# Optimization experiments

Measured on AMD Instinct MI355X. Metric: run time of the kernel, lower is better.

## Reference

```python
import jax, jax.numpy as jnp
import numpy as np
from jax.scipy.special import digamma, gammaln

NUM_CLASSES = 3
FOCAL_GAMMA = 2.0
LABEL_SMOOTHING = 0.1
EVIDENTIAL_W = 0.1
CONTRASTIVE_W = 0.1
BOUNDARY_W = 0.15
TRIPLET_W = 0.1
QUALITY_W = 0.1
TRIPLET_MARGIN = 1.5


def setup_inputs() -> dict:
    key = jax.random.key(0)
    k1, k2, k3 = jax.random.split(key, 3)
    B, D = 4096, 512
    logits = jax.random.normal(k1, (B, NUM_CLASSES), dtype=jnp.float32)
    targets = jax.random.randint(k2, (B,), 0, 3)
    features = jax.random.normal(k3, (B, D), dtype=jnp.float32)
    alpha = jax.random.uniform(jax.random.fold_in(key, 7), (B, NUM_CLASSES), dtype=jnp.float32)
    focal_alpha = jnp.array([1.0, 2.0, 1.5], dtype=jnp.float32)
    class_weights = jnp.array([1.0, 2.0, 1.5], dtype=jnp.float32)
    return {"logits": logits, "targets": targets, "features": features,
            "alpha": alpha, "epoch": 1, "focal_alpha": focal_alpha,
            "class_weights": class_weights}


def reference(logits, targets, features, alpha, epoch, focal_alpha, class_weights):
    B = logits.shape[0]
    C = NUM_CLASSES

    # ---- focal loss (label-smoothed CE, torch semantics) ----
    logp = jax.nn.log_softmax(logits, axis=1)                      # [B,C]
    nll = -jnp.take_along_axis(logp, targets[:, None], axis=1)[:, 0]
    ce_ls = (1.0 - LABEL_SMOOTHING) * nll + LABEL_SMOOTHING * (-logp.mean(axis=1))
    pt = jnp.exp(-ce_ls)
    focal = (focal_alpha[targets] * (1.0 - pt) ** FOCAL_GAMMA * ce_ls).mean()

    # ---- weighted CE (torch weighted mean: sum(w*nll)/sum(w)) ----
    w = class_weights[targets]
    ce = (w * nll).sum() / w.sum()

    # ---- enhanced boundary loss ----
    probs = jax.nn.softmax(logits, axis=1)
    real = targets == 0
    semi = targets == 1
    syn = targets == 2
    rb = jnp.where(real, probs[:, 1] + 0.6 * probs[:, 2], 0.0).sum()
    sb = jnp.where(syn, probs[:, 1] + 0.4 * probs[:, 0], 0.0).sum()
    mb = jnp.where(semi, 1.0 - probs[:, 1] + 0.3 * (probs[:, 0] + probs[:, 2]), 0.0).sum()
    boundary = (rb + sb + 4.5 * mb) / (B + 1e-8)

    total = 0.4 * focal + 0.3 * ce + BOUNDARY_W * boundary

    # ---- normalized features and pairwise cosine-sim matrix ----
    norms = jnp.linalg.norm(features, axis=1, keepdims=True)
    f = features / jnp.maximum(norms, 1e-12)
    sim = f @ f.T                                                  # [B,B]
    same = targets[:, None] == targets[None, :]
    eye = jnp.eye(B, dtype=bool)

    # ---- enhanced contrastive loss ----
    pos = jnp.where(same, (1.0 - sim) ** 2, 0.0).sum()
    neg = jnp.where(~same, jnp.clip(sim - 0.2, 0.0) ** 2, 0.0).sum()
    semi_pair = semi[:, None] & semi[None, :]
    semi_l = jnp.where(semi_pair, (1.0 - sim) ** 2, 0.0).sum()
    contrastive = (pos + neg + 4.0 * semi_l) / (B * B + 1e-8)

    # ---- enhanced triplet loss (batch-hard, vectorized) ----
    d2 = jnp.clip(2.0 - 2.0 * sim, 0.0)
    dist = jnp.sqrt(jnp.where(eye, 1.0, d2))  # diag masked; safe sqrt
    pos_mask = same & ~eye
    neg_mask = ~same
    hp = jnp.max(jnp.where(pos_mask, dist, -jnp.inf), axis=1)
    hn = jnp.min(jnp.where(neg_mask, dist, jnp.inf), axis=1)
    valid = pos_mask.any(axis=1) & neg_mask.any(axis=1)
    margin = TRIPLET_MARGIN * jnp.where(targets == 1, 2.5, 1.0)
    tl = jax.nn.relu(hp - hn + margin)
    cnt = valid.sum()
    triplet = jnp.where(cnt > 0,
                        jnp.where(valid, tl, 0.0).sum() / jnp.maximum(cnt, 1),
                        0.0)

    # ---- quality-invariant loss (upper-tri same-class pairs) ----
    upper = jnp.triu(jnp.ones((B, B), dtype=bool), k=1)
    qmask = same & upper
    npairs = qmask.sum()
    q = jnp.where(qmask, (1.0 - sim) ** 2, 0.0).sum() / jnp.maximum(npairs, 1)
    frac2 = syn.astype(jnp.float32).mean()
    q = q * jnp.where(syn.sum() > 0, 1.0 + 2.5 * frac2, 1.0)
    quality = jnp.where(npairs > 0, q, 0.0)

    # ---- evidential loss ----
    onehot = jax.nn.one_hot(targets, C, dtype=jnp.float32)
    S = alpha.sum(axis=1, keepdims=True) + 1e-8
    likelihood = (onehot * (digamma(S) - digamma(alpha + 1e-8))).sum(axis=1)
    at = onehot + (1.0 - onehot) * alpha
    ats = at.sum(axis=1) + 1e-8
    kl = (gammaln(ats) - gammaln(at + 1e-8).sum(axis=1)
          + ((at - 1.0) * (digamma(at + 1e-8) - digamma(ats[:, None] + 1e-8))).sum(axis=1))
    annealing = min(1.0, (epoch / 25.0) ** 2)
    evidential = likelihood.mean() + annealing * 0.2 * kl.mean()

    total = (total + CONTRASTIVE_W * contrastive + TRIPLET_W * triplet
             + QUALITY_W * quality + EVIDENTIAL_W * evidential)
    return total
```

## Files before the change

kernel.cpp:

```cpp
#include <hip/hip_runtime.h>
#include <hip/hip_bf16.h>
#include <cstdint>

typedef __attribute__((ext_vector_type(8))) __bf16 bf8;
typedef __attribute__((ext_vector_type(4))) float f32x4;

__device__ __forceinline__ unsigned mapf(float x){
  unsigned u = __float_as_uint(x);
  return (u & 0x80000000u) ? ~u : (u | 0x80000000u);
}
__device__ __forceinline__ float unmapf(unsigned u){
  return __uint_as_float((u & 0x80000000u) ? (u & 0x7FFFFFFFu) : ~u);
}

__device__ float digammaf_(float x){
  float r = 0.f;
  while (x < 6.f){ r -= 1.f/x; x += 1.f; }
  float inv = 1.f/x, inv2 = inv*inv;
  r += logf(x) - 0.5f*inv
     - inv2*(0.08333333333f - inv2*(0.008333333333f - inv2*0.003968253968f));
  return r;
}

__global__ __launch_bounds__(256) void k_prep(const float* __restrict__ feat,
    __bf16* __restrict__ fb2,
    const float* __restrict__ logits, const int* __restrict__ targets,
    const float* __restrict__ alpha,  const float* __restrict__ fa,
    const float* __restrict__ cw, int B, int D,
    float* __restrict__ psum, unsigned* rowMinU, unsigned* rowMaxU){
  int bid = blockIdx.x, tid = threadIdx.x;
  int wave = tid >> 6, lane = tid & 63;

  int row = bid*4 + wave;
  const float* src = feat + (size_t)row*D;
  float ss = 0.f;
  for (int c = lane*4; c < D; c += 64*4){
    float4 v = *(const float4*)(src + c);
    ss += v.x*v.x + v.y*v.y + v.z*v.z + v.w*v.w;
  }
  #pragma unroll
  for (int off=32; off; off>>=1) ss += __shfl_xor(ss, off);
  float inv = 1.f / fmaxf(sqrtf(ss), 1e-12f);

  int p = row >> 6, r = row & 63;
  int mi = r >> 4, l16r = r & 15;
  int NCH = D >> 5;
  for (int c = lane*8; c < D; c += 64*8){
    float4 v0 = *(const float4*)(src + c);
    float4 v1 = *(const float4*)(src + c + 4);
    bf8 o;
    o[0]=(__bf16)(v0.x*inv); o[1]=(__bf16)(v0.y*inv);
    o[2]=(__bf16)(v0.z*inv); o[3]=(__bf16)(v0.w*inv);
    o[4]=(__bf16)(v1.x*inv); o[5]=(__bf16)(v1.y*inv);
    o[6]=(__bf16)(v1.z*inv); o[7]=(__bf16)(v1.w*inv);
    int cc = c >> 5;
    int q  = (c >> 3) & 3;
    size_t off = ((size_t)(p*NCH + cc)*4 + mi)*512 + (q*16 + l16r)*8;
    *(bf8*)(fb2 + off) = o;
  }

  if (tid < 4){ rowMinU[bid*4+tid] = 0xFFFFFFFFu; rowMaxU[bid*4+tid] = 0u; }

  if (wave == 0){
    float r0=0.f,r1=0.f,r2=0.f,r3=0.f,r4=0.f,r5=0.f;
    if (lane < 4){
      int i = bid*4 + lane;
      float l0=logits[3*i], l1=logits[3*i+1], l2=logits[3*i+2];
      int t = targets[i];
      float m = fmaxf(l0, fmaxf(l1,l2));
      float e0=expf(l0-m), e1=expf(l1-m), e2=expf(l2-m);
      float se = e0+e1+e2;
      float lse = m + logf(se);
      float lp0=l0-lse, lp1=l1-lse, lp2=l2-lse;
      float lpt = (t==0)?lp0:((t==1)?lp1:lp2);
      float nll = -lpt;
      float ce_ls = 0.9f*nll + 0.1f*(-(lp0+lp1+lp2)*(1.f/3.f));
      float pt = expf(-ce_ls);
      float om = 1.f - pt;
      float focal_i = fa[t]*om*om*ce_ls;
      float w = cw[t];
      float ce_n = w*nll, ce_d = w;
      float p0=e0/se, p1=e1/se, p2=e2/se;
      float bnd;
      if (t==0)      bnd = p1 + 0.6f*p2;
      else if (t==2) bnd = p1 + 0.4f*p0;
      else           bnd = 4.5f*(1.f - p1 + 0.3f*(p0+p2));
      float a0=alpha[3*i], a1=alpha[3*i+1], a2=alpha[3*i+2];
      float S = a0+a1+a2 + 1e-8f;
      float at_ = (t==0)?a0:((t==1)?a1:a2);
      float lik = digammaf_(S) - digammaf_(at_ + 1e-8f);
      float b0 = (t==0)?1.f:a0, b1 = (t==1)?1.f:a1, b2 = (t==2)?1.f:a2;
      float ats = b0+b1+b2 + 1e-8f;
      float psa = digammaf_(ats + 1e-8f);
      float kl = lgammaf(ats)
         - (lgammaf(b0+1e-8f)+lgammaf(b1+1e-8f)+lgammaf(b2+1e-8f))
         + (b0-1.f)*(digammaf_(b0+1e-8f)-psa)
         + (b1-1.f)*(digammaf_(b1+1e-8f)-psa)
         + (b2-1.f)*(digammaf_(b2+1e-8f)-psa);
      r0=focal_i; r1=ce_n; r2=ce_d; r3=bnd; r4=lik; r5=kl;
    }
    float s0 = ((__shfl(r0,0)+__shfl(r0,1))+__shfl(r0,2))+__shfl(r0,3);
    float s1 = ((__shfl(r1,0)+__shfl(r1,1))+__shfl(r1,2))+__shfl(r1,3);
    float s2 = ((__shfl(r2,0)+__shfl(r2,1))+__shfl(r2,2))+__shfl(r2,3);
    float s3 = ((__shfl(r3,0)+__shfl(r3,1))+__shfl(r3,2))+__shfl(r3,3);
    float s4 = ((__shfl(r4,0)+__shfl(r4,1))+__shfl(r4,2))+__shfl(r4,3);
    float s5 = ((__shfl(r5,0)+__shfl(r5,1))+__shfl(r5,2))+__shfl(r5,3);
    if (lane == 0){
      psum[bid*8+0]=s0; psum[bid*8+1]=s1; psum[bid*8+2]=s2;
      psum[bid*8+3]=s3; psum[bid*8+4]=s4; psum[bid*8+5]=s5;
    }
  }
}

__global__ __launch_bounds__(64, 4) void k_pairs(const __bf16* __restrict__ fb2,
    const int* __restrict__ targets, int B, int D,
    float* __restrict__ pairPart, unsigned* rowMinU, unsigned* rowMaxU){
  int NBY = B >> 5;
  int bid = blockIdx.x;
  int by  = bid % NBY;
  int p   = bid / NBY;
  int bx0 = by + 2*p;
  int lane = threadIdx.x;
  if (bx0 >= NBY){
    if (lane == 0) *(float4*)(pairPart + bid*4) = make_float4(0.f,0.f,0.f,0.f);
    return;
  }
  int bx1 = bx0 + 1;
  bool hasT1 = (bx1 < NBY);
  bool isDiag0 = (bx0 == by);
  int rowBase = by*32, colBase0 = bx0*32, colBase1 = bx1*32;

  int quad = lane >> 4, l16 = lane & 15;
  int NCH = D >> 5;

  const __bf16* pA  = fb2 + ((size_t)(by >>1)*NCH*4 + (by &1)*2)*512 + lane*8;
  const __bf16* pB0 = fb2 + ((size_t)(bx0>>1)*NCH*4 + (bx0&1)*2)*512 + lane*8;
  const __bf16* pB1 = hasT1
      ? fb2 + ((size_t)(bx1>>1)*NCH*4 + (bx1&1)*2)*512 + lane*8
      : pB0;

  int trow = targets[rowBase + (lane & 31)];
  int tcol0[2], tcol1[2];
  tcol0[0] = targets[colBase0 + l16];
  tcol0[1] = targets[colBase0 + 16 + l16];
  tcol1[0] = hasT1 ? targets[colBase1 + l16]      : 0;
  tcol1[1] = hasT1 ? targets[colBase1 + 16 + l16] : 0;

  f32x4 C0[2][2] = {};
  f32x4 C1[2][2] = {};

  #define LD(Ab, B0b, B1b, it) do{ \
    Ab[0]  = *(const bf8*)(pA  + (size_t)(it)*2048); \
    Ab[1]  = *(const bf8*)(pA  + (size_t)(it)*2048 + 512); \
    B0b[0] = *(const bf8*)(pB0 + (size_t)(it)*2048); \
    B0b[1] = *(const bf8*)(pB0 + (size_t)(it)*2048 + 512); \
    B1b[0] = *(const bf8*)(pB1 + (size_t)(it)*2048); \
    B1b[1] = *(const bf8*)(pB1 + (size_t)(it)*2048 + 512); \
  }while(0)

  #define COMP(Ab, B0b, B1b) do{ \
    _Pragma("unroll") \
    for (int mi=0; mi<2; mi++) \
      _Pragma("unroll") \
      for (int ni=0; ni<2; ni++) \
        C0[mi][ni] = __builtin_amdgcn_mfma_f32_16x16x32_bf16(Ab[mi], B0b[ni], C0[mi][ni], 0,0,0); \
    _Pragma("unroll") \
    for (int mi=0; mi<2; mi++) \
      _Pragma("unroll") \
      for (int ni=0; ni<2; ni++) \
        C1[mi][ni] = __builtin_amdgcn_mfma_f32_16x16x32_bf16(Ab[mi], B1b[ni], C1[mi][ni], 0,0,0); \
  }while(0)

  if (NCH == 16){
    bf8 A[3][2], Bb0[3][2], Bb1[3][2];
    LD(A[0], Bb0[0], Bb1[0], 0);
    LD(A[1], Bb0[1], Bb1[1], 1);
    #pragma unroll
    for (int it=0; it<16; ++it){
      if (it+2 < 16) LD(A[(it+2)%3], Bb0[(it+2)%3], Bb1[(it+2)%3], it+2);
      COMP(A[it%3], Bb0[it%3], Bb1[it%3]);
    }
  } else {
    bf8 A0[2], B00[2], B10[2], A1[2], B01[2], B11[2];
    LD(A0, B00, B10, 0);
    for (int it=0; it<NCH; it+=2){
      LD(A1, B01, B11, it+1);
      COMP(A0, B00, B10);
      if (it+2 < NCH) LD(A0, B00, B10, it+2);
      COMP(A1, B01, B11);
    }
  }
  #undef LD
  #undef COMP

  float rowMinReg = 2.f, rowMaxReg = -2.f;
  float posA=0.f, negA=0.f, semiA=0.f, diagA=0.f;
  float posB=0.f, negB=0.f, semiB=0.f, diagB=0.f;

  auto epi = [&](const f32x4 (&Cx)[2][2], const int (&tcolx)[2], int colBasex,
                 bool isD, float& posx, float& negx, float& semix, float& diagx){
    float cmin[2] = {2.f, 2.f}, cmax[2] = {-2.f, -2.f};
    #pragma unroll
    for (int mi=0; mi<2; mi++){
      #pragma unroll
      for (int r=0; r<4; r++){
        int rl = mi*16 + quad*4 + r;
        int row = rowBase + rl;
        int tr = __shfl(trow, rl);
        float vmin = 2.f, vmax = -2.f;
        #pragma unroll
        for (int ni=0; ni<2; ni++){
          int col = colBasex + ni*16 + l16;
          float s = Cx[mi][ni][r];
          if (tr == tcolx[ni]){
            float omv = 1.f - s;
            float q = omv*omv;
            posx += q;
            if (tr == 1) semix += q;
            if (row == col) diagx += q;
            else {
              vmin = fminf(vmin, s);
              cmin[ni] = fminf(cmin[ni], s);
            }
          } else {
            float c0 = fmaxf(s - 0.2f, 0.f);
            negx += c0*c0;
            vmax = fmaxf(vmax, s);
            cmax[ni] = fmaxf(cmax[ni], s);
          }
        }
        #pragma unroll
        for (int off=1; off<16; off<<=1){
          vmin = fminf(vmin, __shfl_xor(vmin, off));
          vmax = fmaxf(vmax, __shfl_xor(vmax, off));
        }
        if (l16 == mi*4 + r){
          rowMinReg = fminf(rowMinReg, vmin);
          rowMaxReg = fmaxf(rowMaxReg, vmax);
        }
      }
    }
    if (!isD){
      #pragma unroll
      for (int ni=0; ni<2; ni++){
        cmin[ni] = fminf(cmin[ni], __shfl_xor(cmin[ni], 16));
        cmin[ni] = fminf(cmin[ni], __shfl_xor(cmin[ni], 32));
        cmax[ni] = fmaxf(cmax[ni], __shfl_xor(cmax[ni], 16));
        cmax[ni] = fmaxf(cmax[ni], __shfl_xor(cmax[ni], 32));
      }
      if (lane < 32){
        float cnv = (lane < 16) ? cmin[0] : cmin[1];
        float cxv = (lane < 16) ? cmax[0] : cmax[1];
        atomicMin(&rowMinU[colBasex + lane], mapf(cnv));
        atomicMax(&rowMaxU[colBasex + lane], mapf(cxv));
      }
    }
  };

  epi(C0, tcol0, colBase0, isDiag0, posA, negA, semiA, diagA);
  if (hasT1) epi(C1, tcol1, colBase1, false, posB, negB, semiB, diagB);

  if (l16 < 8){
    int row = rowBase + quad*4 + (l16 & 3) + 16*(l16 >> 2);
    atomicMin(&rowMinU[row], mapf(rowMinReg));
    atomicMax(&rowMaxU[row], mapf(rowMaxReg));
  }

  float fac0 = isDiag0 ? 1.f : 2.f;
  float pos  = posA*fac0 + posB*2.f;
  float neg  = negA*fac0 + negB*2.f;
  float semi = semiA*fac0 + semiB*2.f;
  float diag = diagA;

  #pragma unroll
  for (int off=32; off; off>>=1){
    pos  += __shfl_xor(pos, off);
    neg  += __shfl_xor(neg, off);
    semi += __shfl_xor(semi, off);
    diag += __shfl_xor(diag, off);
  }
  if (lane == 0)
    *(float4*)(pairPart + bid*4) = make_float4(pos, neg, semi, diag);
}

__global__ __launch_bounds__(1024) void k_final(const int* __restrict__ targets,
    const int* __restrict__ epoch_p, int B, int nprep, int nblk,
    const float* __restrict__ pairPart, const float* __restrict__ psum,
    const unsigned* rowMinU, const unsigned* rowMaxU, float* out){
  int tid = threadIdx.x, wave = tid>>6, lane = tid&63;
  __shared__ float redf[16][8];
  __shared__ int   redi[16][4];
  __shared__ float tot6[6];
  __shared__ int   cns[3];
  __shared__ float ptot[4];

  {
    int c0=0,c1=0,c2=0;
    for (int i4 = tid; i4 < B/4; i4 += 1024){
      int4 tv = ((const int4*)targets)[i4];
      c0 += (tv.x==0)+(tv.y==0)+(tv.z==0)+(tv.w==0);
      c1 += (tv.x==1)+(tv.y==1)+(tv.z==1)+(tv.w==1);
      c2 += (tv.x==2)+(tv.y==2)+(tv.z==2)+(tv.w==2);
    }
    #pragma unroll
    for (int off=32; off; off>>=1){
      c0+=__shfl_xor(c0,off); c1+=__shfl_xor(c1,off); c2+=__shfl_xor(c2,off);
    }
    if (lane==0){ redi[wave][0]=c0; redi[wave][1]=c1; redi[wave][2]=c2; }
  }
  {
    float v0=0,v1=0,v2=0,v3=0,v4=0,v5=0;
    for (int s = tid; s < nprep; s += 1024){
      float4 a = *(const float4*)(psum + s*8);
      float4 b = *(const float4*)(psum + s*8 + 4);
      v0+=a.x; v1+=a.y; v2+=a.z; v3+=a.w; v4+=b.x; v5+=b.y;
    }
    #pragma unroll
    for (int off=32; off; off>>=1){
      v0+=__shfl_xor(v0,off); v1+=__shfl_xor(v1,off); v2+=__shfl_xor(v2,off);
      v3+=__shfl_xor(v3,off); v4+=__shfl_xor(v4,off); v5+=__shfl_xor(v5,off);
    }
    if (lane==0){
      redf[wave][0]=v0; redf[wave][1]=v1; redf[wave][2]=v2;
      redf[wave][3]=v3; redf[wave][4]=v4; redf[wave][5]=v5;
    }
  }
  __syncthreads();
  if (tid == 0){
    int c0=0,c1=0,c2=0;
    float v[6]={0,0,0,0,0,0};
    for (int w2=0; w2<16; w2++){
      c0+=redi[w2][0]; c1+=redi[w2][1]; c2+=redi[w2][2];
      for (int j=0;j<6;j++) v[j]+=redf[w2][j];
    }
    cns[0]=c0; cns[1]=c1; cns[2]=c2;
    for (int j=0;j<6;j++) tot6[j]=v[j];
  }
  __syncthreads();

  {
    float p=0,n=0,s2=0,d=0;
    for (int s = tid; s < nblk; s += 1024){
      float4 a = *(const float4*)(pairPart + s*4);
      p+=a.x; n+=a.y; s2+=a.z; d+=a.w;
    }
    #pragma unroll
    for (int off=32; off; off>>=1){
      p+=__shfl_xor(p,off); n+=__shfl_xor(n,off);
      s2+=__shfl_xor(s2,off); d+=__shfl_xor(d,off);
    }
    if (lane==0){ redf[wave][0]=p; redf[wave][1]=n; redf[wave][2]=s2; redf[wave][3]=d; }
  }
  __syncthreads();
  if (tid == 0){
    float a=0,b=0,c=0,e=0;
    for (int w2=0; w2<16; w2++){ a+=redf[w2][0]; b+=redf[w2][1]; c+=redf[w2][2]; e+=redf[w2][3]; }
    ptot[0]=a; ptot[1]=b; ptot[2]=c; ptot[3]=e;
  }
  __syncthreads();

  int n0=cns[0], n1=cns[1], n2=cns[2];

  float tsum = 0.f, tcnt = 0.f;
  for (int i = tid; i < B; i += 1024){
    int t = targets[i];
    int nt = (t==0)?n0:((t==1)?n1:n2);
    if (nt - 1 > 0 && B - nt > 0){
      float mn = unmapf(rowMinU[i]);
      float mx = unmapf(rowMaxU[i]);
      float hp = sqrtf(fmaxf(2.f - 2.f*mn, 0.f));
      float hn = sqrtf(fmaxf(2.f - 2.f*mx, 0.f));
      float margin = 1.5f * ((t==1) ? 2.5f : 1.f);
      float tl = fmaxf(hp - hn + margin, 0.f);
      tsum += tl; tcnt += 1.f;
    }
  }
  #pragma unroll
  for (int off=32; off; off>>=1){ tsum += __shfl_xor(tsum, off); tcnt += __shfl_xor(tcnt, off); }
  if (lane==0){ redf[wave][6]=tsum; redf[wave][7]=tcnt; }
  __syncthreads();

  if (tid==0){
    float ts=0, tn=0;
    for (int w2=0; w2<16; w2++){ ts+=redf[w2][6]; tn+=redf[w2][7]; }
    float triplet = (tn > 0.f) ? ts / fmaxf(tn, 1.f) : 0.f;
    float pos=ptot[0], neg=ptot[1], semi=ptot[2], diag=ptot[3];
    float Bf = (float)B;
    float focal = tot6[0] / Bf;
    float ce = tot6[1] / tot6[2];
    float boundary = tot6[3] / (Bf + 1e-8f);
    float contrastive = (pos + neg + 4.f*semi) / (Bf*Bf + 1e-8f);
    long long npl = ((long long)n0*(n0-1) + (long long)n1*(n1-1) + (long long)n2*(n2-1))/2;
    float qsum = (pos - diag) * 0.5f;
    float q = qsum / (float)(npl > 0 ? npl : 1);
    if (n2 > 0) q *= (1.f + 2.5f * ((float)n2 / Bf));
    float quality = (npl > 0) ? q : 0.f;
    int ep = epoch_p[0];
    float er = (float)ep / 25.f;
    float ann = fminf(1.f, er*er);
    float evidential = tot6[4]/Bf + ann*0.2f*tot6[5]/Bf;
    float total = 0.4f*focal + 0.3f*ce + 0.15f*boundary
                + 0.1f*contrastive + 0.1f*triplet + 0.1f*quality + 0.1f*evidential;
    out[0] = total;
  }
}

extern "C" void kernel_launch(void* const* d_in, const int* in_sizes, int n_in,
                              void* d_out, int out_size, void* d_ws, size_t ws_size,
                              hipStream_t stream){
  const float* logits   = (const float*)d_in[0];
  const int*   targets  = (const int*)d_in[1];
  const float* features = (const float*)d_in[2];
  const float* alpha    = (const float*)d_in[3];
  const int*   epoch    = (const int*)d_in[4];
  const float* fa       = (const float*)d_in[5];
  const float* cw       = (const float*)d_in[6];
  int B = in_sizes[1];
  int D = in_sizes[2] / B;
  int nprep = B/4;
  int NBY = B / 32;
  int PMAX = (NBY + 1) / 2;
  int nblk = NBY * PMAX;

  char* ws = (char*)d_ws;
  float*    psum     = (float*)(ws);
  float*    pairPart = (float*)(ws + 65536);
  unsigned* rowMinU  = (unsigned*)(ws + 65536 + 196608);
  unsigned* rowMaxU  = (unsigned*)(ws + 65536 + 196608 + (size_t)B*4);
  __bf16*   fb2      = (__bf16*)(ws + 65536 + 196608 + (size_t)B*8);

  k_prep <<<nprep, 256, 0, stream>>>(features, fb2, logits, targets, alpha, fa, cw,
                                     B, D, psum, rowMinU, rowMaxU);
  k_pairs<<<nblk, 64, 0, stream>>>(fb2, targets, B, D, pairPart, rowMinU, rowMaxU);
  k_final<<<1, 1024, 0, stream>>>(targets, epoch, B, nprep, nblk, pairPart, psum,
                                  rowMinU, rowMaxU, (float*)d_out);
}
```

Before: 130.1 us.

## Pack four pair-tile waves per block and drop the triple-buffered D=512 path

The pair kernel now launches 256-thread blocks in which each wave handles one independent tile-pair slot, instead of one 64-thread block per slot. This cuts the block count by four and removes the launch bound that allowed four blocks per CU. The specialised triple-buffered, fully unrolled loop for D=512 is removed, so the generic double-buffered loop runs for every D. The aim is to reduce block-scheduling overhead and register pressure, at the risk of hiding memory latency less well in the main loop.

```diff
diff --git a/kernel.cpp b/kernel.cpp
--- a/kernel.cpp
+++ b/kernel.cpp
@@ -112,17 +112,18 @@
   }
 }
 
-__global__ __launch_bounds__(64, 4) void k_pairs(const __bf16* __restrict__ fb2,
-    const int* __restrict__ targets, int B, int D,
+__global__ __launch_bounds__(256) void k_pairs(const __bf16* __restrict__ fb2,
+    const int* __restrict__ targets, int B, int D, int nslot,
     float* __restrict__ pairPart, unsigned* rowMinU, unsigned* rowMaxU){
   int NBY = B >> 5;
-  int bid = blockIdx.x;
-  int by  = bid % NBY;
-  int p   = bid / NBY;
+  int wave = threadIdx.x >> 6, lane = threadIdx.x & 63;
+  int slot = blockIdx.x*4 + wave;
+  if (slot >= nslot) return;
+  int by  = slot % NBY;
+  int p   = slot / NBY;
   int bx0 = by + 2*p;
-  int lane = threadIdx.x;
   if (bx0 >= NBY){
-    if (lane == 0) *(float4*)(pairPart + bid*4) = make_float4(0.f,0.f,0.f,0.f);
+    if (lane == 0) *(float4*)(pairPart + slot*4) = make_float4(0.f,0.f,0.f,0.f);
     return;
   }
   int bx1 = bx0 + 1;
@@ -171,16 +172,7 @@
         C1[mi][ni] = __builtin_amdgcn_mfma_f32_16x16x32_bf16(Ab[mi], B1b[ni], C1[mi][ni], 0,0,0); \
   }while(0)
 
-  if (NCH == 16){
-    bf8 A[3][2], Bb0[3][2], Bb1[3][2];
-    LD(A[0], Bb0[0], Bb1[0], 0);
-    LD(A[1], Bb0[1], Bb1[1], 1);
-    #pragma unroll
-    for (int it=0; it<16; ++it){
-      if (it+2 < 16) LD(A[(it+2)%3], Bb0[(it+2)%3], Bb1[(it+2)%3], it+2);
-      COMP(A[it%3], Bb0[it%3], Bb1[it%3]);
-    }
-  } else {
+  {
     bf8 A0[2], B00[2], B10[2], A1[2], B01[2], B11[2];
     LD(A0, B00, B10, 0);
     for (int it=0; it<NCH; it+=2){
@@ -280,7 +272,7 @@
     diag += __shfl_xor(diag, off);
   }
   if (lane == 0)
-    *(float4*)(pairPart + bid*4) = make_float4(pos, neg, semi, diag);
+    *(float4*)(pairPart + slot*4) = make_float4(pos, neg, semi, diag);
 }
 
 __global__ __launch_bounds__(1024) void k_final(const int* __restrict__ targets,
@@ -420,7 +412,8 @@
   int nprep = B/4;
   int NBY = B / 32;
   int PMAX = (NBY + 1) / 2;
-  int nblk = NBY * PMAX;
+  int nslot = NBY * PMAX;
+  int nblk4 = (nslot + 3) / 4;
 
   char* ws = (char*)d_ws;
   float*    psum     = (float*)(ws);
@@ -431,7 +424,8 @@
 
   k_prep <<<nprep, 256, 0, stream>>>(features, fb2, logits, targets, alpha, fa, cw,
                                      B, D, psum, rowMinU, rowMaxU);
-  k_pairs<<<nblk, 64, 0, stream>>>(fb2, targets, B, D, pairPart, rowMinU, rowMaxU);
-  k_final<<<1, 1024, 0, stream>>>(targets, epoch, B, nprep, nblk, pairPart, psum,
+  k_pairs<<<nblk4, 256, 0, stream>>>(fb2, targets, B, D, nslot, pairPart,
+                                     rowMinU, rowMaxU);
+  k_final<<<1, 1024, 0, stream>>>(targets, epoch, B, nprep, nslot, pairPart, psum,
                                   rowMinU, rowMaxU, (float*)d_out);
 }
```

Result: slower. 137.6 us (+5.8%).
